# Kernel optimization log

Hardware: AMD Instinct MI355X
Metric: run time of the kernel (lower is better)

## Reference

```python
import jax, jax.numpy as jnp
import numpy as np

N_NODES = 50000
N_EDGES = 400000
N_GRAPHS = 64
D_IN = 256
D_HID = 256
D_OUT = 16


def _gcn_conv(x, edge_index, W, b):
    """PyG-style GCNConv: h = D^{-1/2}(A+I)D^{-1/2} (x @ W) + b."""
    n = x.shape[0]
    loop = jnp.arange(n)
    src = jnp.concatenate([edge_index[0], loop])  # [E+N]
    dst = jnp.concatenate([edge_index[1], loop])
    deg = jax.ops.segment_sum(jnp.ones_like(dst, x.dtype), dst, num_segments=n)
    dinv = jnp.where(deg > 0, jax.lax.rsqrt(deg), jnp.zeros_like(deg))
    norm = dinv[src] * dinv[dst]  # [E+N]
    h = x @ W  # linear transform first (as PyG does)
    msg = h[src] * norm[:, None]  # gather + scale, [E+N, D]
    out = jax.ops.segment_sum(msg, dst, num_segments=n)  # scatter-add
    return out + b


def setup_inputs() -> dict:
    key = jax.random.key(0)
    ks = jax.random.split(key, 12)
    x = jax.random.normal(ks[0], (N_NODES, D_IN), dtype=jnp.float32)
    edge_index = jax.random.randint(ks[1], (2, N_EDGES), 0, N_NODES, dtype=jnp.int64)
    batch = jnp.sort(jax.random.randint(ks[2], (N_NODES,), 0, N_GRAPHS, dtype=jnp.int64))

    def glorot(k, fan_in, fan_out):
        s = np.sqrt(6.0 / (fan_in + fan_out)).astype(np.float32)
        return jax.random.uniform(k, (fan_in, fan_out), jnp.float32, -s, s)

    return {
        "x": x,
        "edge_index": edge_index,
        "batch": batch,
        "W1": glorot(ks[3], D_IN, D_HID), "b1": jnp.zeros((D_HID,), jnp.float32),
        "W2": glorot(ks[4], D_HID, D_HID), "b2": jnp.zeros((D_HID,), jnp.float32),
        "W3": glorot(ks[5], D_HID, D_HID), "b3": jnp.zeros((D_HID,), jnp.float32),
        "Wfc": glorot(ks[6], D_HID, D_OUT), "bfc": jnp.zeros((D_OUT,), jnp.float32),
    }


def reference(x, edge_index, batch, W1, b1, W2, b2, W3, b3, Wfc, bfc):
    h = jax.nn.relu(_gcn_conv(x, edge_index, W1, b1))
    h = jax.nn.relu(_gcn_conv(h, edge_index, W2, b2))
    h = jax.nn.relu(_gcn_conv(h, edge_index, W3, b3))
    # global_mean_pool over batch ids
    sums = jax.ops.segment_sum(h, batch, num_segments=N_GRAPHS)  # [G, D]
    cnts = jax.ops.segment_sum(jnp.ones_like(batch, h.dtype), batch, num_segments=N_GRAPHS)
    pooled = sums / jnp.maximum(cnts, 1.0)[:, None]
    return pooled @ Wfc + bfc  # [G, D_OUT]
```

## Files before the change

kernel.cpp:

```cpp
#include <hip/hip_runtime.h>

#define NN 50000
#define NE 400000
#define NG 64
#define D 256
#define DOUT 16

typedef __attribute__((ext_vector_type(8))) short bf16x8;
typedef __attribute__((ext_vector_type(8))) unsigned short u16x8;
typedef __attribute__((ext_vector_type(4))) float f32x4;

__device__ __forceinline__ short f2bf(float x) {
    union { float f; unsigned u; } v; v.f = x;
    unsigned r = v.u + 0x7fffu + ((v.u >> 16) & 1u);
    return (short)(r >> 16);
}
__device__ __forceinline__ float bf2f(short h) {
    union { float f; unsigned u; } v;
    v.u = ((unsigned)(unsigned short)h) << 16;
    return v.f;
}

__device__ __forceinline__ void async_cp16(void* lds, const void* g) {
    __builtin_amdgcn_global_load_lds(
        (const __attribute__((address_space(1))) unsigned int*)g,
        (__attribute__((address_space(3))) unsigned int*)lds, 16, 0, 0);
}


__global__ void k_init(int* __restrict__ cnt, float* __restrict__ pooled,
                       const int* __restrict__ batch, float* __restrict__ inv_cnt,
                       int n) {
    int i = blockIdx.x * 256 + threadIdx.x;
    if (i < n) cnt[i] = 0;
    if (i < NG * D) pooled[i] = 0.f;
    if (blockIdx.x == 0 && threadIdx.x < NG) {
        int g = threadIdx.x;
        int lo = 0, hi = n;
        while (lo < hi) { int mid = (lo + hi) >> 1; if (batch[mid] < g) lo = mid + 1; else hi = mid; }
        int start = lo;
        hi = n;
        while (lo < hi) { int mid = (lo + hi) >> 1; if (batch[mid] < g + 1) lo = mid + 1; else hi = mid; }
        inv_cnt[g] = 1.f / fmaxf((float)(lo - start), 1.f);
    }
}


__global__ void k_split_count(const float* __restrict__ x, unsigned short* __restrict__ ahi,
                              int total4, int xblocks,
                              const float* __restrict__ W1, short* __restrict__ w1hi, short* __restrict__ w1lo,
                              const float* __restrict__ W2, short* __restrict__ w2hi, short* __restrict__ w2lo,
                              const float* __restrict__ W3, short* __restrict__ w3hi, short* __restrict__ w3lo,
                              const int* __restrict__ eidx, int* __restrict__ cnt, int E) {
    int b = blockIdx.x;
    if (b < xblocks) {
        int i = b * 256 + threadIdx.x;
        if (i >= total4) return;
        float4 v = ((const float4*)x)[i];
        ushort4 h;
        h.x = (unsigned short)f2bf(v.x);
        h.y = (unsigned short)f2bf(v.y);
        h.z = (unsigned short)f2bf(v.z);
        h.w = (unsigned short)f2bf(v.w);
        ((ushort4*)ahi)[i] = h;
    } else if (b < xblocks + 3 * 256) {
        int wb = b - xblocks;
        int which = wb >> 8;
        int idx = (wb & 255) * 256 + threadIdx.x;
        int nn = idx >> 8, k = idx & 255;
        const float* W = (which == 0) ? W1 : (which == 1) ? W2 : W3;
        short* Whi = (which == 0) ? w1hi : (which == 1) ? w2hi : w3hi;
        short* Wlo = (which == 0) ? w1lo : (which == 1) ? w2lo : w3lo;
        float xv = W[k * 256 + nn];
        short h = f2bf(xv);
        Whi[idx] = h;
        Wlo[idx] = f2bf(xv - bf2f(h));
    } else {
        int e = (b - xblocks - 3 * 256) * 256 + threadIdx.x;
        if (e < E) atomicAdd(&cnt[eidx[E + e]], 1);
    }
}

__global__ void k_scan1(const int* __restrict__ cnt, int* __restrict__ excl,
                        int* __restrict__ bsums, float* __restrict__ dinv, int n) {
    __shared__ int sh[256];
    int tid = threadIdx.x;
    int base = blockIdx.x * 1024;
    int v[4]; int tsum = 0;
    for (int j = 0; j < 4; ++j) {
        int i = base + tid * 4 + j;
        v[j] = (i < n) ? cnt[i] : 0;
        if (i < n) dinv[i] = rsqrtf((float)(v[j] + 1));
        tsum += v[j];
    }
    sh[tid] = tsum; __syncthreads();
    for (int d = 1; d < 256; d <<= 1) {
        int t = (tid >= d) ? sh[tid - d] : 0;
        __syncthreads();
        sh[tid] += t;
        __syncthreads();
    }
    int run = sh[tid] - tsum;
    for (int j = 0; j < 4; ++j) {
        int i = base + tid * 4 + j;
        if (i < n) excl[i] = run;
        run += v[j];
    }
    if (tid == 255) bsums[blockIdx.x] = sh[255];
}

__global__ void k_scan3(int* __restrict__ row_ptr, const int* __restrict__ bsums,
                        int* __restrict__ cursor, int n, int E, int nb) {
    __shared__ int off_s;
    int chunk = (int)(blockIdx.x >> 2);
    if (threadIdx.x < 64) {
        int v = ((int)threadIdx.x < nb && (int)threadIdx.x < chunk) ? bsums[threadIdx.x] : 0;
        #pragma unroll
        for (int d = 1; d < 64; d <<= 1) v += __shfl_xor(v, d);
        if (threadIdx.x == 0) off_s = v;
    }
    __syncthreads();
    int off = off_s;
    int i = blockIdx.x * 256 + threadIdx.x;
    if (i < n) {
        int v = row_ptr[i] + off;
        row_ptr[i] = v;
        cursor[i] = v;
    }
    if (i == 0) row_ptr[n] = E;
}


__device__ __forceinline__ void gemm_body(
        const unsigned short* __restrict__ A,
        const short* __restrict__ Whi, const short* __restrict__ Wlo,
        const float* __restrict__ dinv, unsigned short* __restrict__ C, int M,
        int bm, short* Ah_s, short* Bh_s, short* Bl_s) {
    const int tid = threadIdx.x;
    const int lane = tid & 63;
    const int w    = tid >> 6;
    const int wm   = w & 1;
    const int wn   = w >> 1;
    const int lm   = lane & 15;
    const int quad = lane >> 4;

    const int srow = tid >> 3, c = tid & 7;
    const int q = c ^ ((srow >> 1) & 7);
    const unsigned short* pa[4];
    #pragma unroll
    for (int j = 0; j < 4; ++j) {
        int ga = bm + j * 32 + srow; if (ga >= M) ga = M - 1;
        pa[j] = A + ((size_t)ga << 8) + q * 8;
    }
    const short* pbh[8]; const short* pbl[8];
    #pragma unroll
    for (int j = 0; j < 8; ++j) {
        pbh[j] = Whi + ((size_t)(j * 32 + srow) << 8) + q * 8;
        pbl[j] = Wlo + ((size_t)(j * 32 + srow) << 8) + q * 8;
    }

    int st[8];
    #pragma unroll
    for (int j = 0; j < 8; ++j) st[j] = j * 2048 + w * 512;

    int oa[4], ob[8];
    #pragma unroll
    for (int i = 0; i < 4; ++i) {
        int ra = wm * 64 + i * 16 + lm;
        oa[i] = ra * 64 + ((quad ^ ((ra >> 1) & 7)) * 8);
    }
    #pragma unroll
    for (int i = 0; i < 8; ++i) {
        int rb = wn * 128 + i * 16 + lm;
        ob[i] = rb * 64 + ((quad ^ ((rb >> 1) & 7)) * 8);
    }

    f32x4 acc[4][8];
    #pragma unroll
    for (int i = 0; i < 4; ++i)
        #pragma unroll
        for (int j = 0; j < 8; ++j)
            acc[i][j] = (f32x4){0.f, 0.f, 0.f, 0.f};

    for (int k0 = 0; k0 < D; k0 += 64) {
        #pragma unroll
        for (int j = 0; j < 4; ++j) async_cp16(&Ah_s[st[j]], pa[j] + k0);
        #pragma unroll
        for (int j = 0; j < 8; ++j) {
            async_cp16(&Bh_s[st[j]], pbh[j] + k0);
            async_cp16(&Bl_s[st[j]], pbl[j] + k0);
        }
        __syncthreads();

        #pragma unroll
        for (int kh = 0; kh < 2; ++kh) {
            const int xo = kh * 32;
            bf16x8 Ah[4], Bh[8], Bl[8];
            #pragma unroll
            for (int i = 0; i < 4; ++i) Ah[i] = *(const bf16x8*)&Ah_s[oa[i] ^ xo];
            #pragma unroll
            for (int i = 0; i < 8; ++i) {
                Bh[i] = *(const bf16x8*)&Bh_s[ob[i] ^ xo];
                Bl[i] = *(const bf16x8*)&Bl_s[ob[i] ^ xo];
            }
            #pragma unroll
            for (int mi = 0; mi < 4; ++mi)
                #pragma unroll
                for (int ni = 0; ni < 8; ++ni) {
                    acc[mi][ni] = __builtin_amdgcn_mfma_f32_16x16x32_bf16(Ah[mi], Bh[ni], acc[mi][ni], 0, 0, 0);
                    acc[mi][ni] = __builtin_amdgcn_mfma_f32_16x16x32_bf16(Ah[mi], Bl[ni], acc[mi][ni], 0, 0, 0);
                }
        }
        __syncthreads();
    }

    #pragma unroll
    for (int mi = 0; mi < 4; ++mi) {
        int rbase = bm + wm * 64 + mi * 16 + quad * 4;
        #pragma unroll
        for (int r = 0; r < 4; ++r) {
            int grow = rbase + r;
            if (grow < M) {
                float s = dinv[grow];
                #pragma unroll
                for (int ni = 0; ni < 8; ++ni) {
                    int col = wn * 128 + ni * 16 + lm;
                    C[(size_t)grow * D + col] = (unsigned short)f2bf(acc[mi][ni][r] * s);
                }
            }
        }
    }
}

__global__ __launch_bounds__(256, 2) void k_gemm_mfma(
        const unsigned short* __restrict__ A,
        const short* __restrict__ Whi, const short* __restrict__ Wlo,
        const float* __restrict__ dinv, unsigned short* __restrict__ C, int M) {
    __shared__ short Ah_s[8192];
    __shared__ short Bh_s[16384];
    __shared__ short Bl_s[16384];
    gemm_body(A, Whi, Wlo, dinv, C, M, blockIdx.x * 128, Ah_s, Bh_s, Bl_s);
}

__global__ __launch_bounds__(256, 2) void k_gemm1_fill(
        const unsigned short* __restrict__ A,
        const short* __restrict__ Whi, const short* __restrict__ Wlo,
        const float* __restrict__ dinv, unsigned short* __restrict__ C, int M,
        int gblocks, const int* __restrict__ eidx, int* __restrict__ cursor,
        int* __restrict__ col_src, int E) {
    __shared__ short Ah_s[8192];
    __shared__ short Bh_s[16384];
    __shared__ short Bl_s[16384];
    if ((int)blockIdx.x < gblocks) {
        gemm_body(A, Whi, Wlo, dinv, C, M, blockIdx.x * 128, Ah_s, Bh_s, Bl_s);
    } else {
        int e = ((int)blockIdx.x - gblocks) * 256 + threadIdx.x;
        if (e < E) {
            int d = eidx[E + e];
            int pos = atomicAdd(&cursor[d], 1);
            col_src[pos] = eidx[e];
        }
    }
}


__global__ __launch_bounds__(256) void k_agg(
        const unsigned short* __restrict__ h, const float* __restrict__ dinv,
        const int* __restrict__ row_ptr, const int* __restrict__ col_src,
        const float* __restrict__ bias,
        unsigned short* __restrict__ ohi, int n) {
    int w = threadIdx.x >> 6, lane = threadIdx.x & 63;
    int node = blockIdx.x * 4 + w;
    if (node >= n) return;
    int half = lane >> 5;
    int dcol = lane & 31;

    float acc[8] = {0.f, 0.f, 0.f, 0.f, 0.f, 0.f, 0.f, 0.f};
    if (half == 0) {
        u16x8 sv = ((const u16x8*)(h + (size_t)node * D))[dcol];
        #pragma unroll
        for (int d = 0; d < 8; ++d) acc[d] = bf2f((short)sv[d]);
    }

    int beg = row_ptr[node], end = row_ptr[node + 1];
    for (int c = beg; c < end; c += 64) {
        int cnt = min(64, end - c);
        int myidx = (lane < cnt) ? col_src[c + lane] : 0;
        for (int e = 0; e < cnt; e += 16) {
            u16x8 u[8];
            bool val[8];
            #pragma unroll
            for (int j = 0; j < 8; ++j) {
                int eid = e + j * 2 + half;
                val[j] = eid < cnt;
                if (val[j]) {
                    int s = __shfl(myidx, eid);
                    u[j] = ((const u16x8*)(h + (size_t)s * D))[dcol];
                }
            }
            #pragma unroll
            for (int j = 0; j < 8; ++j)
                if (val[j]) {
                    #pragma unroll
                    for (int d = 0; d < 8; ++d) acc[d] += bf2f((short)u[j][d]);
                }
        }
    }

    #pragma unroll
    for (int d = 0; d < 8; ++d) acc[d] += __shfl_xor(acc[d], 32);

    if (half == 0) {
        float di = dinv[node];
        float4 b0 = ((const float4*)bias)[dcol * 2];
        float4 b1 = ((const float4*)bias)[dcol * 2 + 1];
        float bb[8] = {b0.x, b0.y, b0.z, b0.w, b1.x, b1.y, b1.z, b1.w};
        u16x8 o;
        #pragma unroll
        for (int d = 0; d < 8; ++d)
            o[d] = (unsigned short)f2bf(fmaxf(acc[d] * di + bb[d], 0.f));
        ((u16x8*)(ohi + (size_t)node * D))[dcol] = o;
    }
}


__global__ __launch_bounds__(256) void k_pool_sum(
        const unsigned short* __restrict__ hi,
        const int* __restrict__ batch, float* __restrict__ pooled, int n) {
    int beg = blockIdx.x * 64;
    if (beg >= n) return;
    int end = min(beg + 64, n);
    int t = threadIdx.x;
    float acc = 0.f;
    int cur = batch[beg];
    for (int i = beg; i < end; ++i) {
        int g = batch[i];
        if (g != cur) {
            atomicAdd(&pooled[cur * D + t], acc);
            acc = 0.f;
            cur = g;
        }
        acc += bf2f(hi[(size_t)i * D + t]);
    }
    atomicAdd(&pooled[cur * D + t], acc);
}


__global__ void k_fc(const float* __restrict__ pooled, const float* __restrict__ inv_cnt,
                     const float* __restrict__ W, const float* __restrict__ b,
                     float* __restrict__ out) {
    int t = blockIdx.x * blockDim.x + threadIdx.x;
    if (t >= NG * DOUT) return;
    int g = t >> 4, o = t & 15;
    float acc = 0.f;
    for (int k = 0; k < D; ++k) acc += pooled[g * D + k] * W[k * DOUT + o];
    out[t] = acc * inv_cnt[g] + b[o];
}


extern "C" void kernel_launch(void* const* d_in, const int* in_sizes, int n_in,
                              void* d_out, int out_size, void* d_ws, size_t ws_size,
                              hipStream_t stream) {
    const float* x    = (const float*)d_in[0];
    const int*   eidx = (const int*)d_in[1];
    const int*   batch= (const int*)d_in[2];
    const float* W1   = (const float*)d_in[3];
    const float* b1   = (const float*)d_in[4];
    const float* W2   = (const float*)d_in[5];
    const float* b2   = (const float*)d_in[6];
    const float* W3   = (const float*)d_in[7];
    const float* b3   = (const float*)d_in[8];
    const float* Wfc  = (const float*)d_in[9];
    const float* bfc  = (const float*)d_in[10];
    float* out = (float*)d_out;

    const int n = in_sizes[0] / D;
    const int E = in_sizes[1] / 2;

    char* p = (char*)d_ws;
    auto take = [&](size_t bytes) -> void* {
        void* q = (void*)p;
        p += (bytes + 255) & ~(size_t)255;
        return q;
    };
    int*   cnt     = (int*)take((size_t)n * 4);
    int*   row_ptr = (int*)take((size_t)(n + 1) * 4);
    int*   cursor  = (int*)take((size_t)n * 4);
    int*   col_src = (int*)take((size_t)E * 4);
    int*   bsums   = (int*)take(256 * 4);
    float* dinv    = (float*)take((size_t)n * 4);
    float* inv_cnt = (float*)take((size_t)NG * 4);
    short* w1hi    = (short*)take((size_t)D * D * 2);
    short* w1lo    = (short*)take((size_t)D * D * 2);
    short* w2hi    = (short*)take((size_t)D * D * 2);
    short* w2lo    = (short*)take((size_t)D * D * 2);
    short* w3hi    = (short*)take((size_t)D * D * 2);
    short* w3lo    = (short*)take((size_t)D * D * 2);
    unsigned short* hbuf = (unsigned short*)take((size_t)n * D * 2);
    unsigned short* ahi  = (unsigned short*)take((size_t)n * D * 2);
    float* pooled  = (float*)take((size_t)NG * D * 4);

    int tb = 256;
    int gn = (n + tb - 1) / tb;
    int ge = (E + tb - 1) / tb;
    int nb = (n + 1023) / 1024;
    int total4 = n * D / 4;
    int xblocks = (total4 + 255) / 256;

    k_init<<<gn, tb, 0, stream>>>(cnt, pooled, batch, inv_cnt, n);
    k_split_count<<<xblocks + 3 * 256 + ge, tb, 0, stream>>>(
        x, ahi, total4, xblocks,
        W1, w1hi, w1lo, W2, w2hi, w2lo, W3, w3hi, w3lo,
        eidx, cnt, E);
    k_scan1<<<nb, 256, 0, stream>>>(cnt, row_ptr, bsums, dinv, n);
    k_scan3<<<gn, tb, 0, stream>>>(row_ptr, bsums, cursor, n, E, nb);

    int ggrid = (n + 127) / 128;
    int agrid = (n + 3) / 4;

    k_gemm1_fill<<<ggrid + ge, 256, 0, stream>>>(ahi, w1hi, w1lo, dinv, hbuf, n,
                                                 ggrid, eidx, cursor, col_src, E);
    k_agg<<<agrid, 256, 0, stream>>>(hbuf, dinv, row_ptr, col_src, b1, ahi, n);

    k_gemm_mfma<<<ggrid, 256, 0, stream>>>(ahi, w2hi, w2lo, dinv, hbuf, n);
    k_agg<<<agrid, 256, 0, stream>>>(hbuf, dinv, row_ptr, col_src, b2, ahi, n);

    k_gemm_mfma<<<ggrid, 256, 0, stream>>>(ahi, w3hi, w3lo, dinv, hbuf, n);
    k_agg<<<agrid, 256, 0, stream>>>(hbuf, dinv, row_ptr, col_src, b3, ahi, n);

    k_pool_sum<<<(n + 63) / 64, 256, 0, stream>>>(ahi, batch, pooled, n);
    k_fc<<<4, 256, 0, stream>>>(pooled, inv_cnt, Wfc, bfc, out);
}
```

Baseline: 358.5 us.

## Switch activations and weights to fp16 and drop the split-weight GEMM

Activations, intermediate features and weights now use fp16 instead of bf16. The weight hi/lo split is removed, so each GEMM does a single fp16 MFMA per tile instead of two bf16 MFMAs, and the weight load traffic is halved. The GEMM tile is reduced from 128 to 64 rows with each wave covering 64 columns, LDS use drops, and the occupancy hint rises from 2 to 3 blocks. The extra fp16 mantissa bits are meant to make up for the lost compensation term, but fp16's smaller range risks overflow or precision loss that bf16 would not have.

New measurement: 349.2 us. 1.03x faster.

```diff
diff --git a/kernel.cpp b/kernel.cpp
--- a/kernel.cpp
+++ b/kernel.cpp
@@ -6,19 +6,19 @@
 #define D 256
 #define DOUT 16
 
-typedef __attribute__((ext_vector_type(8))) short bf16x8;
+typedef __attribute__((ext_vector_type(8))) _Float16 f16x8;
 typedef __attribute__((ext_vector_type(8))) unsigned short u16x8;
 typedef __attribute__((ext_vector_type(4))) float f32x4;
 
-__device__ __forceinline__ short f2bf(float x) {
-    union { float f; unsigned u; } v; v.f = x;
-    unsigned r = v.u + 0x7fffu + ((v.u >> 16) & 1u);
-    return (short)(r >> 16);
-}
-__device__ __forceinline__ float bf2f(short h) {
-    union { float f; unsigned u; } v;
-    v.u = ((unsigned)(unsigned short)h) << 16;
-    return v.f;
+__device__ __forceinline__ unsigned short f2h(float x) {
+    union { _Float16 h; unsigned short u; } v;
+    v.h = (_Float16)x;
+    return v.u;
+}
+__device__ __forceinline__ float h2f(unsigned short u) {
+    union { _Float16 h; unsigned short u; } v;
+    v.u = u;
+    return (float)v.h;
 }
 
 __device__ __forceinline__ void async_cp16(void* lds, const void* g) {
@@ -48,9 +48,9 @@
 
 __global__ void k_split_count(const float* __restrict__ x, unsigned short* __restrict__ ahi,
                               int total4, int xblocks,
-                              const float* __restrict__ W1, short* __restrict__ w1hi, short* __restrict__ w1lo,
-                              const float* __restrict__ W2, short* __restrict__ w2hi, short* __restrict__ w2lo,
-                              const float* __restrict__ W3, short* __restrict__ w3hi, short* __restrict__ w3lo,
+                              const float* __restrict__ W1, short* __restrict__ w1h,
+                              const float* __restrict__ W2, short* __restrict__ w2h,
+                              const float* __restrict__ W3, short* __restrict__ w3h,
                               const int* __restrict__ eidx, int* __restrict__ cnt, int E) {
     int b = blockIdx.x;
     if (b < xblocks) {
@@ -58,10 +58,10 @@
         if (i >= total4) return;
         float4 v = ((const float4*)x)[i];
         ushort4 h;
-        h.x = (unsigned short)f2bf(v.x);
-        h.y = (unsigned short)f2bf(v.y);
-        h.z = (unsigned short)f2bf(v.z);
-        h.w = (unsigned short)f2bf(v.w);
+        h.x = f2h(v.x);
+        h.y = f2h(v.y);
+        h.z = f2h(v.z);
+        h.w = f2h(v.w);
         ((ushort4*)ahi)[i] = h;
     } else if (b < xblocks + 3 * 256) {
         int wb = b - xblocks;
@@ -69,12 +69,8 @@
         int idx = (wb & 255) * 256 + threadIdx.x;
         int nn = idx >> 8, k = idx & 255;
         const float* W = (which == 0) ? W1 : (which == 1) ? W2 : W3;
-        short* Whi = (which == 0) ? w1hi : (which == 1) ? w2hi : w3hi;
-        short* Wlo = (which == 0) ? w1lo : (which == 1) ? w2lo : w3lo;
-        float xv = W[k * 256 + nn];
-        short h = f2bf(xv);
-        Whi[idx] = h;
-        Wlo[idx] = f2bf(xv - bf2f(h));
+        short* Wh = (which == 0) ? w1h : (which == 1) ? w2h : w3h;
+        Wh[idx] = (short)f2h(W[k * 256 + nn]);
     } else {
         int e = (b - xblocks - 3 * 256) * 256 + threadIdx.x;
         if (e < E) atomicAdd(&cnt[eidx[E + e]], 1);
@@ -133,126 +129,110 @@
 
 __device__ __forceinline__ void gemm_body(
         const unsigned short* __restrict__ A,
-        const short* __restrict__ Whi, const short* __restrict__ Wlo,
+        const short* __restrict__ Wh,
         const float* __restrict__ dinv, unsigned short* __restrict__ C, int M,
-        int bm, short* Ah_s, short* Bh_s, short* Bl_s) {
+        int bm, short* Ah_s, short* Bh_s) {
     const int tid = threadIdx.x;
     const int lane = tid & 63;
     const int w    = tid >> 6;
-    const int wm   = w & 1;
-    const int wn   = w >> 1;
     const int lm   = lane & 15;
     const int quad = lane >> 4;
 
     const int srow = tid >> 3, c = tid & 7;
     const int q = c ^ ((srow >> 1) & 7);
-    const unsigned short* pa[4];
-    #pragma unroll
-    for (int j = 0; j < 4; ++j) {
+    const unsigned short* pa[2];
+    #pragma unroll
+    for (int j = 0; j < 2; ++j) {
         int ga = bm + j * 32 + srow; if (ga >= M) ga = M - 1;
         pa[j] = A + ((size_t)ga << 8) + q * 8;
     }
-    const short* pbh[8]; const short* pbl[8];
-    #pragma unroll
-    for (int j = 0; j < 8; ++j) {
-        pbh[j] = Whi + ((size_t)(j * 32 + srow) << 8) + q * 8;
-        pbl[j] = Wlo + ((size_t)(j * 32 + srow) << 8) + q * 8;
-    }
+    const short* pbh[8];
+    #pragma unroll
+    for (int j = 0; j < 8; ++j)
+        pbh[j] = Wh + ((size_t)(j * 32 + srow) << 8) + q * 8;
 
     int st[8];
     #pragma unroll
     for (int j = 0; j < 8; ++j) st[j] = j * 2048 + w * 512;
 
-    int oa[4], ob[8];
+    int oa[4], ob[4];
     #pragma unroll
     for (int i = 0; i < 4; ++i) {
-        int ra = wm * 64 + i * 16 + lm;
+        int ra = i * 16 + lm;
         oa[i] = ra * 64 + ((quad ^ ((ra >> 1) & 7)) * 8);
-    }
-    #pragma unroll
-    for (int i = 0; i < 8; ++i) {
-        int rb = wn * 128 + i * 16 + lm;
+        int rb = w * 64 + i * 16 + lm;
         ob[i] = rb * 64 + ((quad ^ ((rb >> 1) & 7)) * 8);
     }
 
-    f32x4 acc[4][8];
+    f32x4 acc[4][4];
     #pragma unroll
     for (int i = 0; i < 4; ++i)
         #pragma unroll
-        for (int j = 0; j < 8; ++j)
+        for (int j = 0; j < 4; ++j)
             acc[i][j] = (f32x4){0.f, 0.f, 0.f, 0.f};
 
     for (int k0 = 0; k0 < D; k0 += 64) {
         #pragma unroll
-        for (int j = 0; j < 4; ++j) async_cp16(&Ah_s[st[j]], pa[j] + k0);
-        #pragma unroll
-        for (int j = 0; j < 8; ++j) {
-            async_cp16(&Bh_s[st[j]], pbh[j] + k0);
-            async_cp16(&Bl_s[st[j]], pbl[j] + k0);
-        }
+        for (int j = 0; j < 2; ++j) async_cp16(&Ah_s[st[j]], pa[j] + k0);
+        #pragma unroll
+        for (int j = 0; j < 8; ++j) async_cp16(&Bh_s[st[j]], pbh[j] + k0);
         __syncthreads();
 
         #pragma unroll
         for (int kh = 0; kh < 2; ++kh) {
             const int xo = kh * 32;
-            bf16x8 Ah[4], Bh[8], Bl[8];
+            f16x8 Ah[4], Bh[4];
             #pragma unroll
-            for (int i = 0; i < 4; ++i) Ah[i] = *(const bf16x8*)&Ah_s[oa[i] ^ xo];
-            #pragma unroll
-            for (int i = 0; i < 8; ++i) {
-                Bh[i] = *(const bf16x8*)&Bh_s[ob[i] ^ xo];
-                Bl[i] = *(const bf16x8*)&Bl_s[ob[i] ^ xo];
+            for (int i = 0; i < 4; ++i) {
+                Ah[i] = *(const f16x8*)&Ah_s[oa[i] ^ xo];
+                Bh[i] = *(const f16x8*)&Bh_s[ob[i] ^ xo];
             }
             #pragma unroll
             for (int mi = 0; mi < 4; ++mi)
                 #pragma unroll
-                for (int ni = 0; ni < 8; ++ni) {
-                    acc[mi][ni] = __builtin_amdgcn_mfma_f32_16x16x32_bf16(Ah[mi], Bh[ni], acc[mi][ni], 0, 0, 0);
-                    acc[mi][ni] = __builtin_amdgcn_mfma_f32_16x16x32_bf16(Ah[mi], Bl[ni], acc[mi][ni], 0, 0, 0);
-                }
+                for (int ni = 0; ni < 4; ++ni)
+                    acc[mi][ni] = __builtin_amdgcn_mfma_f32_16x16x32_f16(Ah[mi], Bh[ni], acc[mi][ni], 0, 0, 0);
         }
         __syncthreads();
     }
 
     #pragma unroll
     for (int mi = 0; mi < 4; ++mi) {
-        int rbase = bm + wm * 64 + mi * 16 + quad * 4;
+        int rbase = bm + mi * 16 + quad * 4;
         #pragma unroll
         for (int r = 0; r < 4; ++r) {
             int grow = rbase + r;
             if (grow < M) {
                 float s = dinv[grow];
                 #pragma unroll
-                for (int ni = 0; ni < 8; ++ni) {
-                    int col = wn * 128 + ni * 16 + lm;
-                    C[(size_t)grow * D + col] = (unsigned short)f2bf(acc[mi][ni][r] * s);
+                for (int ni = 0; ni < 4; ++ni) {
+                    int col = w * 64 + ni * 16 + lm;
+                    C[(size_t)grow * D + col] = f2h(acc[mi][ni][r] * s);
                 }
             }
         }
     }
 }
 
-__global__ __launch_bounds__(256, 2) void k_gemm_mfma(
+__global__ __launch_bounds__(256, 3) void k_gemm_mfma(
         const unsigned short* __restrict__ A,
-        const short* __restrict__ Whi, const short* __restrict__ Wlo,
+        const short* __restrict__ Wh,
         const float* __restrict__ dinv, unsigned short* __restrict__ C, int M) {
-    __shared__ short Ah_s[8192];
+    __shared__ short Ah_s[4096];
     __shared__ short Bh_s[16384];
-    __shared__ short Bl_s[16384];
-    gemm_body(A, Whi, Wlo, dinv, C, M, blockIdx.x * 128, Ah_s, Bh_s, Bl_s);
-}
-
-__global__ __launch_bounds__(256, 2) void k_gemm1_fill(
+    gemm_body(A, Wh, dinv, C, M, blockIdx.x * 64, Ah_s, Bh_s);
+}
+
+__global__ __launch_bounds__(256, 3) void k_gemm1_fill(
         const unsigned short* __restrict__ A,
-        const short* __restrict__ Whi, const short* __restrict__ Wlo,
+        const short* __restrict__ Wh,
         const float* __restrict__ dinv, unsigned short* __restrict__ C, int M,
         int gblocks, const int* __restrict__ eidx, int* __restrict__ cursor,
         int* __restrict__ col_src, int E) {
-    __shared__ short Ah_s[8192];
+    __shared__ short Ah_s[4096];
     __shared__ short Bh_s[16384];
-    __shared__ short Bl_s[16384];
     if ((int)blockIdx.x < gblocks) {
-        gemm_body(A, Whi, Wlo, dinv, C, M, blockIdx.x * 128, Ah_s, Bh_s, Bl_s);
+        gemm_body(A, Wh, dinv, C, M, blockIdx.x * 64, Ah_s, Bh_s);
     } else {
         int e = ((int)blockIdx.x - gblocks) * 256 + threadIdx.x;
         if (e < E) {
@@ -279,7 +259,7 @@
     if (half == 0) {
         u16x8 sv = ((const u16x8*)(h + (size_t)node * D))[dcol];
         #pragma unroll
-        for (int d = 0; d < 8; ++d) acc[d] = bf2f((short)sv[d]);
+        for (int d = 0; d < 8; ++d) acc[d] = h2f(sv[d]);
     }
 
     int beg = row_ptr[node], end = row_ptr[node + 1];
@@ -302,7 +282,7 @@
             for (int j = 0; j < 8; ++j)
                 if (val[j]) {
                     #pragma unroll
-                    for (int d = 0; d < 8; ++d) acc[d] += bf2f((short)u[j][d]);
+                    for (int d = 0; d < 8; ++d) acc[d] += h2f(u[j][d]);
                 }
         }
     }
@@ -318,7 +298,7 @@
         u16x8 o;
         #pragma unroll
         for (int d = 0; d < 8; ++d)
-            o[d] = (unsigned short)f2bf(fmaxf(acc[d] * di + bb[d], 0.f));
+            o[d] = f2h(fmaxf(acc[d] * di + bb[d], 0.f));
         ((u16x8*)(ohi + (size_t)node * D))[dcol] = o;
     }
 }
@@ -340,7 +320,7 @@
             acc = 0.f;
             cur = g;
         }
-        acc += bf2f(hi[(size_t)i * D + t]);
+        acc += h2f(hi[(size_t)i * D + t]);
     }
     atomicAdd(&pooled[cur * D + t], acc);
 }
@@ -390,12 +370,9 @@
     int*   bsums   = (int*)take(256 * 4);
     float* dinv    = (float*)take((size_t)n * 4);
     float* inv_cnt = (float*)take((size_t)NG * 4);
-    short* w1hi    = (short*)take((size_t)D * D * 2);
-    short* w1lo    = (short*)take((size_t)D * D * 2);
-    short* w2hi    = (short*)take((size_t)D * D * 2);
-    short* w2lo    = (short*)take((size_t)D * D * 2);
-    short* w3hi    = (short*)take((size_t)D * D * 2);
-    short* w3lo    = (short*)take((size_t)D * D * 2);
+    short* w1h     = (short*)take((size_t)D * D * 2);
+    short* w2h     = (short*)take((size_t)D * D * 2);
+    short* w3h     = (short*)take((size_t)D * D * 2);
     unsigned short* hbuf = (unsigned short*)take((size_t)n * D * 2);
     unsigned short* ahi  = (unsigned short*)take((size_t)n * D * 2);
     float* pooled  = (float*)take((size_t)NG * D * 4);
@@ -410,22 +387,22 @@
     k_init<<<gn, tb, 0, stream>>>(cnt, pooled, batch, inv_cnt, n);
     k_split_count<<<xblocks + 3 * 256 + ge, tb, 0, stream>>>(
         x, ahi, total4, xblocks,
-        W1, w1hi, w1lo, W2, w2hi, w2lo, W3, w3hi, w3lo,
+        W1, w1h, W2, w2h, W3, w3h,
         eidx, cnt, E);
     k_scan1<<<nb, 256, 0, stream>>>(cnt, row_ptr, bsums, dinv, n);
     k_scan3<<<gn, tb, 0, stream>>>(row_ptr, bsums, cursor, n, E, nb);
 
-    int ggrid = (n + 127) / 128;
+    int ggrid = (n + 63) / 64;
     int agrid = (n + 3) / 4;
 
-    k_gemm1_fill<<<ggrid + ge, 256, 0, stream>>>(ahi, w1hi, w1lo, dinv, hbuf, n,
+    k_gemm1_fill<<<ggrid + ge, 256, 0, stream>>>(ahi, w1h, dinv, hbuf, n,
                                                  ggrid, eidx, cursor, col_src, E);
     k_agg<<<agrid, 256, 0, stream>>>(hbuf, dinv, row_ptr, col_src, b1, ahi, n);
 
-    k_gemm_mfma<<<ggrid, 256, 0, stream>>>(ahi, w2hi, w2lo, dinv, hbuf, n);
+    k_gemm_mfma<<<ggrid, 256, 0, stream>>>(ahi, w2h, dinv, hbuf, n);
     k_agg<<<agrid, 256, 0, stream>>>(hbuf, dinv, row_ptr, col_src, b2, ahi, n);
 
-    k_gemm_mfma<<<ggrid, 256, 0, stream>>>(ahi, w3hi, w3lo, dinv, hbuf, n);
+    k_gemm_mfma<<<ggrid, 256, 0, stream>>>(ahi, w3h, dinv, hbuf, n);
     k_agg<<<agrid, 256, 0, stream>>>(hbuf, dinv, row_ptr, col_src, b3, ahi, n);
 
     k_pool_sum<<<(n + 63) / 64, 256, 0, stream>>>(ahi, batch, pooled, n);
```
